# Optimization experiments

Hardware: AMD Instinct MI355X
Metric: run time of the kernel (lower is better)

The kernel has to match this reference:

```python
import jax, jax.numpy as jnp
import numpy as np

X, Y, Z, E, K, ITERS = 128, 128, 8, 64, 3, 3
XYZ = X * Y * Z
IMG_H, IMG_W = 384, 1280
FH, FW = 96, 320  # img_feat spatial size
LN_EPS = 1e-5
GRAD_SCALE = 0.1


def _homo_grid():
    # get_coordinates: meshgrid(arange(x), -arange(y), arange(z)), then append ones
    xs = (np.arange(X) * 0.8 + 0.0).astype(np.float32)
    ys = (-(np.arange(Y) * 0.8 - 51.2)).astype(np.float32)
    zs = (np.arange(Z) * 0.5 - 2.5).astype(np.float32)
    gx, gy, gz = np.meshgrid(xs, ys, zs, indexing='ij')
    g = np.stack([gx, gy, gz, np.ones_like(gx)], axis=-1)  # (X,Y,Z,4)
    return jnp.asarray(g)


def _grid_sample(img, grid):
    # F.grid_sample: bilinear, padding_mode='zeros', align_corners=False
    # img: (B,C,H,W), grid: (B,N,K,2) xy in [-1,1] -> out (B,C,N,K)
    B, C, H, W = img.shape
    x = ((grid[..., 0] + 1.0) * W - 1.0) * 0.5
    y = ((grid[..., 1] + 1.0) * H - 1.0) * 0.5
    x0 = jnp.floor(x); y0 = jnp.floor(y)
    x1 = x0 + 1.0; y1 = y0 + 1.0
    wx1 = x - x0; wx0 = 1.0 - wx1
    wy1 = y - y0; wy0 = 1.0 - wy1
    flat = img.reshape(B, C, H * W)

    def gather(xi, yi):
        valid = (xi >= 0) & (xi < W) & (yi >= 0) & (yi < H)  # (B,N,K)
        xi_c = jnp.clip(xi, 0, W - 1).astype(jnp.int32)
        yi_c = jnp.clip(yi, 0, H - 1).astype(jnp.int32)
        idx = yi_c * W + xi_c  # (B,N,K)
        g = jnp.take_along_axis(flat, idx.reshape(B, 1, -1), axis=2)
        g = g.reshape(B, C, idx.shape[1], idx.shape[2])
        return g * valid[:, None].astype(img.dtype)

    out = (gather(x0, y0) * (wx0 * wy0)[:, None]
           + gather(x1, y0) * (wx1 * wy0)[:, None]
           + gather(x0, y1) * (wx0 * wy1)[:, None]
           + gather(x1, y1) * (wx1 * wy1)[:, None])
    return out


def setup_inputs() -> dict:
    key = jax.random.key(0)
    ks = jax.random.split(key, 8)
    # realistic extrinsic (velo->cam) and intrinsic so projections land in-image
    T_velo2cam = jnp.array([[[0., -1., 0., 0.],
                             [0., 0., -1., -0.3],
                             [1., 0., 0., 0.5]]], dtype=jnp.float32)
    intrinsic = jnp.array([[[700., 0., 640.],
                            [0., 700., 192.],
                            [0., 0., 1.]]], dtype=jnp.float32)
    img_feat = jax.random.normal(ks[0], (1, E, FH, FW), jnp.float32)
    bev_embedding = 0.1 * jax.random.normal(ks[1], (X, Y, Z, E), jnp.float32)
    W_off = 0.02 * jax.random.normal(ks[2], (ITERS, E, 2 * K), jnp.float32)
    b_off = 0.02 * jax.random.normal(ks[3], (ITERS, 2 * K), jnp.float32)
    s_off = jnp.full((ITERS,), 0.1, jnp.float32)  # Scale(0.1)
    W_w = 0.02 * jax.random.normal(ks[4], (ITERS, E, K), jnp.float32)
    b_w = jnp.zeros((ITERS, K), jnp.float32)
    W_l = (E ** -0.5) * jax.random.normal(ks[5], (ITERS, E, E), jnp.float32)
    b_l = jnp.zeros((ITERS, E), jnp.float32)
    ln_g = jnp.ones((ITERS, E), jnp.float32)
    ln_b = jnp.zeros((ITERS, E), jnp.float32)
    return dict(T_velo2cam=T_velo2cam, intrinsic=intrinsic, img_feat=img_feat,
                bev_embedding=bev_embedding, W_off=W_off, b_off=b_off, s_off=s_off,
                W_w=W_w, b_w=b_w, W_l=W_l, b_l=b_l, ln_g=ln_g, ln_b=ln_b)


def reference(T_velo2cam, intrinsic, img_feat, bev_embedding,
              W_off, b_off, s_off, W_w, b_w, W_l, b_l, ln_g, ln_b):
    homo = _homo_grid()  # (X,Y,Z,4)
    T = jnp.einsum('bij,bjk->bik', intrinsic, T_velo2cam)  # (B,3,4)
    pts = jnp.einsum('bij,xyzj->bxyzi', T, homo)  # (B,X,Y,Z,3)
    uv = pts[..., 0:2] / pts[..., 2:3]
    half = jnp.array([IMG_W / 2.0, IMG_H / 2.0], pts.dtype)
    coord = (uv / half - 1.0).reshape(1, XYZ, 1, 2)  # (B,XYZ,1,2)
    bev = bev_embedding.reshape(1, XYZ, 1, E)
    for i in range(ITERS):
        off = (bev @ W_off[i] + b_off[i]) * s_off[i]  # Linear -> Scale
        # GradientScale(0.1): identity fwd, grad*0.1 bwd
        off = GRAD_SCALE * off + jax.lax.stop_gradient((1.0 - GRAD_SCALE) * off)
        off = off.reshape(1, XYZ, K, 2)
        w = jax.nn.softmax(bev @ W_w[i] + b_w[i], axis=-1)[:, :, 0, :]  # (1,XYZ,K)
        feat = _grid_sample(img_feat, coord + off)  # (1,E,XYZ,K)
        feat = jnp.sum(feat * w[:, None], axis=-1)  # (1,E,XYZ)
        bev = bev + jnp.transpose(feat, (0, 2, 1))[:, :, None, :]  # (1,XYZ,1,E)
        # LinearLNDropout (dropout inactive in eval)
        h = bev @ W_l[i] + b_l[i]
        mu = jnp.mean(h, axis=-1, keepdims=True)
        var = jnp.mean((h - mu) ** 2, axis=-1, keepdims=True)
        h = (h - mu) * jax.lax.rsqrt(var + LN_EPS) * ln_g[i] + ln_b[i]
        bev = bev + h
    bev = bev.reshape(1, X, Y, Z, E)
    return jnp.transpose(bev, (0, 4, 2, 1, 3)).mean(-1)  # (B,E,Y,X)
```

## Files before the change

### kernel.cpp

```cpp
#include <hip/hip_runtime.h>
#include <math.h>

#define XD 128
#define YD 128
#define ZD 8
#define ED 64
#define KD 3
#define NITER 3
#define FHD 96
#define FWD 320
#define HALF_W 640.0f
#define HALF_H 192.0f

#define ASTRIDE 80
#define DSTR 28
#define HSTR 68

#define WAVE_LDS 4352

typedef __attribute__((ext_vector_type(8))) short short8;
typedef __attribute__((ext_vector_type(4))) float f32x4;
typedef float          __attribute__((may_alias)) fal;
typedef unsigned       __attribute__((may_alias)) ual;
typedef unsigned short __attribute__((may_alias)) usal;

__device__ __forceinline__ unsigned short f2bf(float f) {
    unsigned u = __float_as_uint(f);
    u += 0x7fff + ((u >> 16) & 1);
    return (unsigned short)(u >> 16);
}

__device__ __forceinline__ int pk2bf(float a, float b) {
    return (int)((unsigned)f2bf(a) | ((unsigned)f2bf(b) << 16));
}

__device__ __forceinline__ float dot2bf(float acc, unsigned a, int b) {
#if defined(__has_builtin) && __has_builtin(__builtin_amdgcn_fdot2_f32_bf16)
    typedef __bf16 bf16x2 __attribute__((ext_vector_type(2)));
    union U { unsigned u; bf16x2 v; };
    U ua, ub;
    ua.u = a;
    ub.u = (unsigned)b;
    return __builtin_amdgcn_fdot2_f32_bf16(ua.v, ub.v, acc, false);
#else
    asm("v_dot2_f32_bf16 %0, %1, %2, %0" : "+v"(acc) : "v"(a), "s"(b));
    return acc;
#endif
}

__device__ __forceinline__ float rowsum16(float v) {
    v += __int_as_float(__builtin_amdgcn_update_dpp(0, __float_as_int(v), 0x121, 0xf, 0xf, true));
    v += __int_as_float(__builtin_amdgcn_update_dpp(0, __float_as_int(v), 0x122, 0xf, 0xf, true));
    v += __int_as_float(__builtin_amdgcn_update_dpp(0, __float_as_int(v), 0x124, 0xf, 0xf, true));
    v += __int_as_float(__builtin_amdgcn_update_dpp(0, __float_as_int(v), 0x128, 0xf, 0xf, true));
    return v;
}

__global__ __launch_bounds__(256) void k_prep(const float* __restrict__ img,
                                              unsigned* __restrict__ imgP,
                                              const float* __restrict__ W_off,
                                              const float* __restrict__ W_w,
                                              const float* __restrict__ W_l,
                                              unsigned short* __restrict__ W9f,
                                              unsigned short* __restrict__ Wlf) {
    if (blockIdx.x < (FHD * FWD) / 64) {
        __shared__ float tile[64][65];
        const int hw0 = blockIdx.x * 64;
        const int lane = threadIdx.x & 63;
        const int r = threadIdx.x >> 6;
#pragma unroll
        for (int i = 0; i < 16; ++i) {
            int e = r + 4 * i;
            tile[e][lane] = img[e * (FHD * FWD) + hw0 + lane];
        }
        __syncthreads();
        const bool edge_block = ((hw0 % FWD) == FWD - 64);
#pragma unroll
        for (int i = 0; i < 16; ++i) {
            int row = r + 4 * i;
            float v1 = tile[lane][row];
            float v2;
            if (row < 63) {
                v2 = tile[lane][row + 1];
            } else {
                v2 = edge_block ? 0.0f : img[lane * (FHD * FWD) + hw0 + 64];
            }
            imgP[(hw0 + row) * 64 + lane] =
                (unsigned)f2bf(v1) | ((unsigned)f2bf(v2) << 16);
        }
    } else {
        int idx = (blockIdx.x - (FHD * FWD) / 64) * 256 + threadIdx.x;
        if (idx < 3 * 4 * 2 * 64) {
            int lane = idx & 63, s = (idx >> 6) & 1, t = (idx >> 7) & 3, i = idx >> 9;
            int n = t * 16 + (lane & 15), quad = lane >> 4;
#pragma unroll
            for (int jj = 0; jj < 8; ++jj) {
                int ep = s * 32 + quad * 8 + jj;
                Wlf[idx * 8 + jj] = f2bf(W_l[(i * ED + ep) * ED + n]);
            }
        } else if (idx < 3 * 4 * 2 * 64 + 3 * 2 * 64) {
            int k = idx - 3 * 4 * 2 * 64;
            int lane = k & 63, s = (k >> 6) & 1, i = k >> 7;
            int n = lane & 15, quad = lane >> 4;
#pragma unroll
            for (int jj = 0; jj < 8; ++jj) {
                int ep = s * 32 + quad * 8 + jj;
                float v = 0.0f;
                if (n < 6) v = W_off[(i * ED + ep) * 6 + n];
                else if (n < 9) v = W_w[(i * ED + ep) * 3 + (n - 6)];
                W9f[k * 8 + jj] = f2bf(v);
            }
        }
    }
}

__global__ __launch_bounds__(256, 4) void k_main(
    const float* __restrict__ Tv,
    const float* __restrict__ intr,
    const unsigned* __restrict__ imgP,
    const float* __restrict__ bev_in,
    const unsigned short* __restrict__ W9f,
    const unsigned short* __restrict__ Wlf,
    const float* __restrict__ b_off,
    const float* __restrict__ s_off,
    const float* __restrict__ b_w,
    const float* __restrict__ b_l,
    const float* __restrict__ ln_g,
    const float* __restrict__ ln_b,
    float* __restrict__ tmp)
{
    __shared__ __align__(16) char smem[4 * WAVE_LDS];

    const int lane = threadIdx.x & 63;
    const int wv = threadIdx.x >> 6;
    const int b = blockIdx.x;
    const int blkS = ((b & 7) << 8) | (b >> 3);
    const int wid2 = __builtin_amdgcn_readfirstlane(blkS * 4 + wv);
    const int m16 = lane & 15;
    const int quad = lane >> 4;

    char* base = smem + wv * WAVE_LDS;
    usal* Ab = (usal*)base;
    fal*  Db = (fal*)base;
    fal*  Hb = (fal*)base;

    const char* imgB = (const char*)imgP;

    float T[12];
#pragma unroll
    for (int r = 0; r < 3; ++r)
#pragma unroll
        for (int c = 0; c < 4; ++c)
            T[r * 4 + c] = intr[r * 3 + 0] * Tv[0 * 4 + c] +
                           intr[r * 3 + 1] * Tv[1 * 4 + c] +
                           intr[r * 3 + 2] * Tv[2 * 4 + c];

    const int sm = min(lane / 3, 15);
    const int sk = lane - (lane / 3) * 3;

    float cxd, cyd;
    {
        int p = sm >> 3, z = sm & 7;
        int q = 2 * wid2 + p;
        int x = q & (XD - 1);
        int y = q >> 7;
        float gx = x * 0.8f;
        float gy = 51.2f - y * 0.8f;
        float gz = z * 0.5f - 2.5f;
        float p0 = T[0] * gx + T[1] * gy + T[2] * gz + T[3];
        float p1 = T[4] * gx + T[5] * gy + T[6] * gz + T[7];
        float p2 = T[8] * gx + T[9] * gy + T[10] * gz + T[11];
        cxd = (p0 / p2) / HALF_W - 1.0f;
        cyd = (p1 / p2) / HALF_H - 1.0f;
    }

    float bev[16];
#pragma unroll
    for (int p = 0; p < 2; ++p) {
        int q = 2 * wid2 + p;
        int x = q & (XD - 1);
        int y = q >> 7;
        int pbase = (((x << 7) | y) << 9);
#pragma unroll
        for (int z = 0; z < ZD; ++z)
            bev[p * 8 + z] = bev_in[pbase + z * ED + lane];
    }

    for (int i = 0; i < NITER; ++i) {
#pragma unroll
        for (int m = 0; m < 16; ++m) Ab[m * ASTRIDE + lane] = f2bf(bev[m]);

        short8 wb0 = *(const short8*)(W9f + ((i * 2 + 0) * 64 + lane) * 8);
        short8 wb1 = *(const short8*)(W9f + ((i * 2 + 1) * 64 + lane) * 8);
        short8 a0 = *(const short8*)(Ab + m16 * ASTRIDE + quad * 8);
        short8 a1 = *(const short8*)(Ab + m16 * ASTRIDE + 32 + quad * 8);
        f32x4 dlog = {0.0f, 0.0f, 0.0f, 0.0f};
        dlog = __builtin_amdgcn_mfma_f32_16x16x32_bf16(a0, wb0, dlog, 0, 0, 0);
        dlog = __builtin_amdgcn_mfma_f32_16x16x32_bf16(a1, wb1, dlog, 0, 0, 0);
#pragma unroll
        for (int r = 0; r < 4; ++r) Db[(quad * 4 + r) * DSTR + m16] = dlog[r];

        const float so = s_off[i];
        const float bo0 = b_off[i * 6 + 0], bo1 = b_off[i * 6 + 1], bo2 = b_off[i * 6 + 2];
        const float bo3 = b_off[i * 6 + 3], bo4 = b_off[i * 6 + 4], bo5 = b_off[i * 6 + 5];
        const float bw0 = b_w[i * 3 + 0], bw1 = b_w[i * 3 + 1], bw2 = b_w[i * 3 + 2];

        int rowAB;
        int w01, w23;
        {
            const fal* Dm = Db + sm * DSTR;
            f32x4 qa = *(const f32x4*)(Dm);
            f32x4 qb = *(const f32x4*)(Dm + 4);
            float l8 = Dm[8];

            float ox0 = (qa[0] + bo0) * so, oy0 = (qa[1] + bo1) * so;
            float ox1 = (qa[2] + bo2) * so, oy1 = (qa[3] + bo3) * so;
            float ox2 = (qb[0] + bo4) * so, oy2 = (qb[1] + bo5) * so;
            float l0 = qb[2] + bw0, l1 = qb[3] + bw1, l2 = l8 + bw2;
            float mx = fmaxf(fmaxf(l0, l1), l2);
            float e0 = __expf(l0 - mx), e1 = __expf(l1 - mx), e2 = __expf(l2 - mx);
            float inv = 1.0f / (e0 + e1 + e2);
            float wk0 = e0 * inv, wk1 = e1 * inv, wk2 = e2 * inv;

            float wkk = (sk == 0) ? wk0 : ((sk == 1) ? wk1 : wk2);
            float ox  = (sk == 0) ? ox0 : ((sk == 1) ? ox1 : ox2);
            float oy  = (sk == 0) ? oy0 : ((sk == 1) ? oy1 : oy2);

            float gxx = cxd + ox, gyy = cyd + oy;
            float px = ((gxx + 1.0f) * (float)FWD - 1.0f) * 0.5f;
            float py = ((gyy + 1.0f) * (float)FHD - 1.0f) * 0.5f;
            float x0f = floorf(px), y0f = floorf(py);
            float fx = px - x0f, fy = py - y0f;
            int ix0 = (int)x0f, iy0 = (int)y0f;
            int iy1 = iy0 + 1;

            int cb = min(max(ix0, 0), FWD - 1);
            float wA = (ix0 >= 0 && ix0 < FWD) ? (1.0f - fx)
                                               : ((ix0 == -1) ? fx : 0.0f);
            float wB = (ix0 >= 0 && ix0 + 1 < FWD) ? fx : 0.0f;

            int rb0 = min(max(iy0, 0), FHD - 1);
            int rb1 = min(max(iy1, 0), FHD - 1);
            float wy0v = (iy0 >= 0 && iy0 < FHD) ? (1.0f - fy) : 0.0f;
            float wy1v = (iy1 >= 0 && iy1 < FHD) ? fy : 0.0f;

            rowAB = (rb0 * FWD + cb) | ((rb1 * FWD + cb) << 16);
            w01 = pk2bf(wkk * wA * wy0v, wkk * wB * wy0v);
            w23 = pk2bf(wkk * wA * wy1v, wkk * wB * wy1v);
        }

        float b2[16];
#pragma unroll
        for (int m = 0; m < 16; ++m) {
            float fA = 0.0f, fB = 0.0f;
#pragma unroll
            for (int k = 0; k < KD; ++k) {
                const int s = m * 3 + k;
                unsigned rAB = (unsigned)__builtin_amdgcn_readlane(rowAB, s);
                int wa = __builtin_amdgcn_readlane(w01, s);
                int wb = __builtin_amdgcn_readlane(w23, s);
                size_t offA = (size_t)(rAB & 0xffffu) << 8;
                size_t offB = (size_t)(rAB >> 16) << 8;
                const ual* pA = (const ual*)(imgB + offA) + lane;
                const ual* pB = (const ual*)(imgB + offB) + lane;
                unsigned uA = *pA, uB = *pB;
                fA = dot2bf(fA, uA, wa);
                fB = dot2bf(fB, uB, wb);
            }
            b2[m] = bev[m] + (fA + fB);
        }

#pragma unroll
        for (int m = 0; m < 16; ++m) Ab[m * ASTRIDE + lane] = f2bf(b2[m]);
        short8 a0b = *(const short8*)(Ab + m16 * ASTRIDE + quad * 8);
        short8 a1b = *(const short8*)(Ab + m16 * ASTRIDE + 32 + quad * 8);
        f32x4 accs[4];
#pragma unroll
        for (int t = 0; t < 4; ++t) {
            float bb = b_l[i * ED + t * 16 + m16];
            f32x4 acc = {bb, bb, bb, bb};
            short8 w0 = *(const short8*)(Wlf + (((i * 4 + t) * 2 + 0) * 64 + lane) * 8);
            short8 w1 = *(const short8*)(Wlf + (((i * 4 + t) * 2 + 1) * 64 + lane) * 8);
            acc = __builtin_amdgcn_mfma_f32_16x16x32_bf16(a0b, w0, acc, 0, 0, 0);
            acc = __builtin_amdgcn_mfma_f32_16x16x32_bf16(a1b, w1, acc, 0, 0, 0);
            accs[t] = acc;
        }

        float s1[4], s2[4];
#pragma unroll
        for (int r = 0; r < 4; ++r) {
            s1[r] = accs[0][r] + accs[1][r] + accs[2][r] + accs[3][r];
            s2[r] = accs[0][r] * accs[0][r];
            s2[r] = fmaf(accs[1][r], accs[1][r], s2[r]);
            s2[r] = fmaf(accs[2][r], accs[2][r], s2[r]);
            s2[r] = fmaf(accs[3][r], accs[3][r], s2[r]);
            s1[r] = rowsum16(s1[r]);
            s2[r] = rowsum16(s2[r]);
        }
        float gt[4], bt[4];
#pragma unroll
        for (int t = 0; t < 4; ++t) {
            gt[t] = ln_g[i * ED + t * 16 + m16];
            bt[t] = ln_b[i * ED + t * 16 + m16];
        }
#pragma unroll
        for (int r = 0; r < 4; ++r) {
            float mu = s1[r] * (1.0f / 64.0f);
            float var = fmaxf(s2[r] * (1.0f / 64.0f) - mu * mu, 0.0f);
            float rs = rsqrtf(var + 1e-5f);
            int row = quad * 4 + r;
#pragma unroll
            for (int t = 0; t < 4; ++t) {
                float hn = (accs[t][r] - mu) * rs * gt[t] + bt[t];
                Hb[row * HSTR + t * 16 + m16] = hn;
            }
        }
#pragma unroll
        for (int m = 0; m < 16; ++m) bev[m] = b2[m] + Hb[m * HSTR + lane];
    }

#pragma unroll
    for (int p = 0; p < 2; ++p) {
        float s = 0.0f;
#pragma unroll
        for (int z = 0; z < ZD; ++z) s += bev[p * 8 + z];
        tmp[(2 * wid2 + p) * ED + lane] = s * 0.125f;
    }
}

__global__ __launch_bounds__(256) void k_transpose(const float* __restrict__ tmp,
                                                   float* __restrict__ out) {
    __shared__ float tile[64][65];
    const int p0 = blockIdx.x * 64;
    const int lane = threadIdx.x & 63;
    const int r = threadIdx.x >> 6;
#pragma unroll
    for (int i = 0; i < 16; ++i) {
        int row = r + 4 * i;
        tile[row][lane] = tmp[(p0 + row) * ED + lane];
    }
    __syncthreads();
#pragma unroll
    for (int i = 0; i < 16; ++i) {
        int erow = r + 4 * i;
        out[erow * (YD * XD) + p0 + lane] = tile[lane][erow];
    }
}

extern "C" void kernel_launch(void* const* d_in, const int* in_sizes, int n_in,
                              void* d_out, int out_size, void* d_ws, size_t ws_size,
                              hipStream_t stream) {
    const float* Tv      = (const float*)d_in[0];
    const float* intr    = (const float*)d_in[1];
    const float* img     = (const float*)d_in[2];
    const float* bev_in  = (const float*)d_in[3];
    const float* W_off   = (const float*)d_in[4];
    const float* b_off   = (const float*)d_in[5];
    const float* s_off   = (const float*)d_in[6];
    const float* W_w     = (const float*)d_in[7];
    const float* b_w     = (const float*)d_in[8];
    const float* W_l     = (const float*)d_in[9];
    const float* b_l     = (const float*)d_in[10];
    const float* ln_g    = (const float*)d_in[11];
    const float* ln_b    = (const float*)d_in[12];
    float* out = (float*)d_out;

    char* ws = (char*)d_ws;
    unsigned* imgP = (unsigned*)ws;
    float* tmp = (float*)(ws + 7864320);
    unsigned short* W9f = (unsigned short*)(ws + 7864320 + 4194304);
    unsigned short* Wlf = (unsigned short*)(ws + 7864320 + 4194304 + 6144);

    k_prep<<<(FHD * FWD) / 64 + 8, 256, 0, stream>>>(img, imgP, W_off, W_w, W_l,
                                                     W9f, Wlf);
    k_main<<<(XD * YD / 2) / 4, 256, 0, stream>>>(Tv, intr, imgP, bev_in,
                                                  W9f, Wlf, b_off, s_off, b_w,
                                                  b_l, ln_g, ln_b, tmp);
    k_transpose<<<(YD * XD) / 64, 256, 0, stream>>>(tmp, out);
}
```

Measured before the change: 147.8 us.

## Use hardware bf16 pack conversion, raise occupancy, and stagger block starts

Replaces the software round-to-nearest bf16 conversion with the HIP packed float2-to-bfloat162 intrinsic, which can map to a hardware packed convert instruction. It also raises the launch-bounds occupancy hint from 4 to 8 blocks per CU, which caps registers per thread. Finally it adds an s_sleep delay at block start that grows with block index, to spread the gather traffic over time. The stagger adds idle time, and the tighter register limit risks spills.

```diff
diff --git a/kernel.cpp b/kernel.cpp
--- a/kernel.cpp
+++ b/kernel.cpp
@@ -1,4 +1,5 @@
 #include <hip/hip_runtime.h>
+#include <hip/hip_bf16.h>
 #include <math.h>
 
 #define XD 128
@@ -30,8 +31,17 @@
     return (unsigned short)(u >> 16);
 }
 
+__device__ __forceinline__ unsigned pk2bf_hw(float a, float b) {
+    union { __hip_bfloat162 h; unsigned u; } cv;
+    float2 f;
+    f.x = a;
+    f.y = b;
+    cv.h = __float22bfloat162_rn(f);
+    return cv.u;
+}
+
 __device__ __forceinline__ int pk2bf(float a, float b) {
-    return (int)((unsigned)f2bf(a) | ((unsigned)f2bf(b) << 16));
+    return (int)pk2bf_hw(a, b);
 }
 
 __device__ __forceinline__ float dot2bf(float acc, unsigned a, int b) {
@@ -114,7 +124,7 @@
     }
 }
 
-__global__ __launch_bounds__(256, 4) void k_main(
+__global__ __launch_bounds__(256, 8) void k_main(
     const float* __restrict__ Tv,
     const float* __restrict__ intr,
     const unsigned* __restrict__ imgP,
@@ -139,6 +149,15 @@
     const int m16 = lane & 15;
     const int quad = lane >> 4;
 
+    {
+        int gen = (b >> 8) & 7;
+        for (int j = 0; j < gen; ++j) {
+            __builtin_amdgcn_s_sleep(15);
+            __builtin_amdgcn_s_sleep(15);
+            __builtin_amdgcn_s_sleep(8);
+        }
+    }
+
     char* base = smem + wv * WAVE_LDS;
     usal* Ab = (usal*)base;
     fal*  Db = (fal*)base;
@@ -188,7 +207,11 @@
 
     for (int i = 0; i < NITER; ++i) {
 #pragma unroll
-        for (int m = 0; m < 16; ++m) Ab[m * ASTRIDE + lane] = f2bf(bev[m]);
+        for (int m = 0; m < 16; m += 2) {
+            unsigned u = pk2bf_hw(bev[m], bev[m + 1]);
+            Ab[m * ASTRIDE + lane] = (usal)u;
+            Ab[(m + 1) * ASTRIDE + lane] = (usal)(u >> 16);
+        }
 
         short8 wb0 = *(const short8*)(W9f + ((i * 2 + 0) * 64 + lane) * 8);
         short8 wb1 = *(const short8*)(W9f + ((i * 2 + 1) * 64 + lane) * 8);
@@ -271,7 +294,11 @@
         }
 
 #pragma unroll
-        for (int m = 0; m < 16; ++m) Ab[m * ASTRIDE + lane] = f2bf(b2[m]);
+        for (int m = 0; m < 16; m += 2) {
+            unsigned u = pk2bf_hw(b2[m], b2[m + 1]);
+            Ab[m * ASTRIDE + lane] = (usal)u;
+            Ab[(m + 1) * ASTRIDE + lane] = (usal)(u >> 16);
+        }
         short8 a0b = *(const short8*)(Ab + m16 * ASTRIDE + quad * 8);
         short8 a1b = *(const short8*)(Ab + m16 * ASTRIDE + 32 + quad * 8);
         f32x4 accs[4];
```

Result: slower. 154.0 us (+4.2%).
